# Kernel optimization log

Measured on AMD Instinct MI355X. Metric: run time of the kernel, lower is better.

## Reference

```python
import jax, jax.numpy as jnp
import numpy as np

OBS_LEN = 20   # decoder timesteps
NC = 2         # n_coordinates
D = 64         # z_dim + s_dim (LSTM hidden size)
K = 20         # number of latent samples (len(pred_lstm_hidden))
N = 50000      # number of agents
H_MID = 32     # mapping MLP hidden dim


def setup_inputs() -> dict:
    key = jax.random.key(0)
    ks = jax.random.split(key, 8)
    return {
        "obs_traj_rel": jax.random.normal(ks[0], (OBS_LEN, N, NC), jnp.float32),
        "pred_lstm_hidden": jax.random.normal(ks[1], (K, N, D), jnp.float32),
        # mapping MLP: Linear(D->32) + LeakyReLU, Linear(32->D)
        "map_w1": jax.random.normal(ks[2], (H_MID, D), jnp.float32) * 0.1,
        "map_b1": jnp.zeros((H_MID,), jnp.float32),
        "map_w2": jax.random.normal(ks[3], (D, H_MID), jnp.float32) * 0.1,
        "map_b2": jnp.zeros((D,), jnp.float32),
        # LSTMCell params (weights ~ N(0, 0.1), biases zero per _initialize_weights)
        "w_ih": jax.random.normal(ks[4], (4 * D, NC), jnp.float32) * 0.1,
        "w_hh": jax.random.normal(ks[5], (4 * D, D), jnp.float32) * 0.1,
        "b_ih": jnp.zeros((4 * D,), jnp.float32),
        "b_hh": jnp.zeros((4 * D,), jnp.float32),
        # pred_hidden2pos: Linear(D -> NC)
        "pos_w": jax.random.normal(ks[6], (NC, D), jnp.float32) * 0.1,
        "pos_b": jnp.zeros((NC,), jnp.float32),
    }


def _hardsigmoid(x):
    # F.hardsigmoid: relu6(x + 3) / 6
    return jnp.clip(x / 6.0 + 0.5, 0.0, 1.0)


def _hardtanh(x):
    return jnp.clip(x, -1.0, 1.0)


def reference(obs_traj_rel, pred_lstm_hidden, map_w1, map_b1, map_w2, map_b2,
              w_ih, w_hh, b_ih, b_hh, pos_w, pos_b):
    # mapping MLP on initial hidden state: [K, N, D]
    h0 = jax.nn.leaky_relu(pred_lstm_hidden @ map_w1.T + map_b1, negative_slope=0.01)
    h0 = h0 @ map_w2.T + map_b2
    c0 = jnp.zeros_like(h0)

    # input at step i uses obs_traj_rel[max(i-1, 0)]
    idx = jnp.concatenate([jnp.zeros((1,), jnp.int32),
                           jnp.arange(OBS_LEN - 1, dtype=jnp.int32)])
    xs = obs_traj_rel[idx, :, :NC]  # [T, N, NC]

    def step(carry, x_t):
        h, c = carry                                   # [K, N, D]
        xb = jnp.broadcast_to(x_t, (K,) + x_t.shape)   # repeat over samples
        gates = xb @ w_ih.T + b_ih + h @ w_hh.T + b_hh  # [K, N, 4D]
        i_g, f_g, g_g, o_g = jnp.split(gates, 4, axis=-1)
        c_new = _hardsigmoid(f_g) * c + _hardsigmoid(i_g) * _hardtanh(g_g)
        h_new = _hardsigmoid(o_g) * _hardtanh(c_new)
        out = h_new @ pos_w.T + pos_b                  # [K, N, NC]
        return (h_new, c_new), out

    _, outs = jax.lax.scan(step, (h0, c0), xs)
    return outs  # [T, K, N, NC]
```

## Files before the change

kernel.cpp:

```cpp
#include <hip/hip_runtime.h>

#define T_STEPS 20
#define KK      20
#define NW      50000
#define DD      64

typedef __attribute__((ext_vector_type(8))) short bfx8;
typedef __attribute__((ext_vector_type(4))) short sx4;
typedef __attribute__((ext_vector_type(4))) float fx4;

__device__ __forceinline__ short f2bf(float f){
  unsigned u = __builtin_bit_cast(unsigned, f);
  return (short)((u + 0x7FFFu + ((u >> 16) & 1u)) >> 16);
}
__device__ __forceinline__ float hsig(float x){ return fminf(fmaxf(fmaf(x, 0.16666667f, 0.5f), 0.f), 1.f); }
__device__ __forceinline__ float htanh(float x){ return fminf(fmaxf(x, -1.f), 1.f); }

__device__ __forceinline__ bfx8 frag_f32(const float* p0, const float* p1){
  fx4 lo = *(const fx4*)p0, hi = *(const fx4*)p1;
  bfx8 r;
  r[0]=f2bf(lo[0]); r[1]=f2bf(lo[1]); r[2]=f2bf(lo[2]); r[3]=f2bf(lo[3]);
  r[4]=f2bf(hi[0]); r[5]=f2bf(hi[1]); r[6]=f2bf(hi[2]); r[7]=f2bf(hi[3]);
  return r;
}
__device__ __forceinline__ bfx8 frag_lds(const unsigned short* p0, const unsigned short* p1){
  sx4 lo = *(const sx4*)p0, hi = *(const sx4*)p1;
  bfx8 r;
  r[0]=lo[0]; r[1]=lo[1]; r[2]=lo[2]; r[3]=lo[3];
  r[4]=hi[0]; r[5]=hi[1]; r[6]=hi[2]; r[7]=hi[3];
  return r;
}

__global__ __launch_bounds__(256)
void gcrl_fused(const float* __restrict__ obs, const float* __restrict__ pred,
                const float* __restrict__ w1, const float* __restrict__ b1,
                const float* __restrict__ w2, const float* __restrict__ b2,
                const float* __restrict__ wih, const float* __restrict__ whh,
                const float* __restrict__ bih, const float* __restrict__ bhh,
                const float* __restrict__ posw, const float* __restrict__ posb,
                float* __restrict__ out)
{
  __shared__ unsigned short hbuf[2][16][72];
  __shared__ unsigned short l1buf[16][36];
  __shared__ float xs[19][4][2];

  const int tid = threadIdx.x;
  const int w   = tid >> 6;
  const int l   = tid & 63;
  const int g   = l >> 4;
  const int cc  = l & 15;

  const int bid = blockIdx.x;
  const int k0  = (bid % 5) * 4;
  const int n0  = (bid / 5) * 4;

  for (int i = tid; i < 19 * 8; i += 256){
    int row = i >> 3, r = i & 7;
    xs[row][r >> 1][r & 1] = obs[(size_t)row * (NW * 2) + (size_t)(n0 + (r >> 1)) * 2 + (r & 1)];
  }

  bfx8 wf[4][2];
  float wx0[4], wx1[4], bsum[4];
  #pragma unroll
  for (int ty = 0; ty < 4; ++ty){
    const int j = ty * 64 + w * 16 + cc;
    wx0[ty]  = wih[j * 2 + 0];
    wx1[ty]  = wih[j * 2 + 1];
    bsum[ty] = bih[j] + bhh[j];
    #pragma unroll
    for (int kt = 0; kt < 2; ++kt)
      wf[ty][kt] = frag_f32(&whh[j * DD + kt * 32 + g * 4],
                            &whh[j * DD + kt * 32 + 16 + g * 4]);
  }

  const int c2 = (cc < 2) ? cc : 0;
  bfx8 pf[2];
  #pragma unroll
  for (int kt = 0; kt < 2; ++kt)
    pf[kt] = frag_f32(&posw[c2 * DD + kt * 32 + g * 4],
                      &posw[c2 * DD + kt * 32 + 16 + g * 4]);
  const float pbias = posb[c2];

  {
    const int kcell = k0 + (cc & 3);
    const int ncell = n0 + (cc >> 2);
    const float* Pr = pred + ((size_t)kcell * NW + ncell) * DD;
    bfx8 pa0 = frag_f32(&Pr[g * 4],      &Pr[16 + g * 4]);
    bfx8 pa1 = frag_f32(&Pr[32 + g * 4], &Pr[48 + g * 4]);
    if (w == 0){
      #pragma unroll
      for (int nt = 0; nt < 2; ++nt){
        const int j1 = nt * 16 + cc;
        bfx8 bf0 = frag_f32(&w1[j1 * DD + g * 4],      &w1[j1 * DD + 16 + g * 4]);
        bfx8 bf1 = frag_f32(&w1[j1 * DD + 32 + g * 4], &w1[j1 * DD + 48 + g * 4]);
        const float bb = b1[j1];
        fx4 acc = {bb, bb, bb, bb};
        acc = __builtin_amdgcn_mfma_f32_16x16x32_bf16(pa0, bf0, acc, 0, 0, 0);
        acc = __builtin_amdgcn_mfma_f32_16x16x32_bf16(pa1, bf1, acc, 0, 0, 0);
        #pragma unroll
        for (int r = 0; r < 4; ++r){
          float xv = acc[r];
          l1buf[g * 4 + r][nt * 16 + cc] =
            (unsigned short)f2bf(fmaxf(xv, 0.f) + 0.01f * fminf(xv, 0.f));
        }
      }
    }
  }
  __syncthreads();
  {
    bfx8 a2 = frag_lds(&l1buf[cc][g * 4], &l1buf[cc][16 + g * 4]);
    const int j2 = w * 16 + cc;
    bfx8 b2f = frag_f32(&w2[j2 * 32 + g * 4], &w2[j2 * 32 + 16 + g * 4]);
    const float bb = b2[j2];
    fx4 acc = {bb, bb, bb, bb};
    acc = __builtin_amdgcn_mfma_f32_16x16x32_bf16(a2, b2f, acc, 0, 0, 0);
    #pragma unroll
    for (int r = 0; r < 4; ++r)
      hbuf[0][g * 4 + r][w * 16 + cc] = (unsigned short)f2bf(acc[r]);
  }
  float cst[4] = {0.f, 0.f, 0.f, 0.f};
  __syncthreads();

  #pragma unroll 2
  for (int t = 0; t < T_STEPS; ++t){
    const int xi = (t == 0) ? 0 : (t - 1);
    const float x0v = xs[xi][g][0];
    const float x1v = xs[xi][g][1];

    const unsigned short* hrow = &hbuf[t & 1][cc][0];
    bfx8 ha0 = frag_lds(&hrow[g * 4],      &hrow[16 + g * 4]);
    bfx8 ha1 = frag_lds(&hrow[32 + g * 4], &hrow[48 + g * 4]);

    fx4 acc[4];
    #pragma unroll
    for (int ty = 0; ty < 4; ++ty){
      const float xv = fmaf(wx0[ty], x0v, fmaf(wx1[ty], x1v, bsum[ty]));
      fx4 a = {xv, xv, xv, xv};
      a = __builtin_amdgcn_mfma_f32_16x16x32_bf16(ha0, wf[ty][0], a, 0, 0, 0);
      a = __builtin_amdgcn_mfma_f32_16x16x32_bf16(ha1, wf[ty][1], a, 0, 0, 0);
      acc[ty] = a;
    }

    if (w == 0 && t > 0){
      fx4 oa = {pbias, pbias, pbias, pbias};
      oa = __builtin_amdgcn_mfma_f32_16x16x32_bf16(ha0, pf[0], oa, 0, 0, 0);
      oa = __builtin_amdgcn_mfma_f32_16x16x32_bf16(ha1, pf[1], oa, 0, 0, 0);
      if (cc < 2){
        #pragma unroll
        for (int r = 0; r < 4; ++r)
          out[(((size_t)(t - 1) * KK + (k0 + r)) * NW + (n0 + g)) * 2 + cc] = oa[r];
      }
    }

    #pragma unroll
    for (int r = 0; r < 4; ++r){
      const float iv = acc[0][r], fv = acc[1][r], gv = acc[2][r], ov = acc[3][r];
      const float cn = fmaf(hsig(fv), cst[r], hsig(iv) * htanh(gv));
      cst[r] = cn;
      hbuf[(t + 1) & 1][g * 4 + r][w * 16 + cc] = (unsigned short)f2bf(hsig(ov) * htanh(cn));
    }
    __syncthreads();
  }

  if (w == 0){
    const unsigned short* hrow = &hbuf[0][cc][0];
    bfx8 ha0 = frag_lds(&hrow[g * 4],      &hrow[16 + g * 4]);
    bfx8 ha1 = frag_lds(&hrow[32 + g * 4], &hrow[48 + g * 4]);
    fx4 oa = {pbias, pbias, pbias, pbias};
    oa = __builtin_amdgcn_mfma_f32_16x16x32_bf16(ha0, pf[0], oa, 0, 0, 0);
    oa = __builtin_amdgcn_mfma_f32_16x16x32_bf16(ha1, pf[1], oa, 0, 0, 0);
    if (cc < 2){
      #pragma unroll
      for (int r = 0; r < 4; ++r)
        out[(((size_t)19 * KK + (k0 + r)) * NW + (n0 + g)) * 2 + cc] = oa[r];
    }
  }
}

extern "C" void kernel_launch(void* const* d_in, const int* in_sizes, int n_in,
                              void* d_out, int out_size, void* d_ws, size_t ws_size,
                              hipStream_t stream){
  const float* obs  = (const float*)d_in[0];
  const float* pred = (const float*)d_in[1];
  const float* w1   = (const float*)d_in[2];
  const float* b1   = (const float*)d_in[3];
  const float* w2   = (const float*)d_in[4];
  const float* b2   = (const float*)d_in[5];
  const float* wih  = (const float*)d_in[6];
  const float* whh  = (const float*)d_in[7];
  const float* bih  = (const float*)d_in[8];
  const float* bhh  = (const float*)d_in[9];
  const float* posw = (const float*)d_in[10];
  const float* posb = (const float*)d_in[11];
  float* o = (float*)d_out;

  dim3 grid((NW / 4) * (KK / 4));
  dim3 block(256);
  gcrl_fused<<<grid, block, 0, stream>>>(obs, pred, w1, b1, w2, b2,
                                         wih, whh, bih, bhh, posw, posb, o);
}
```

Baseline: 1.279 ms.

## Process two cell tiles per block with transposed MFMA and packed bf16 LDS traffic

Each block now covers 8 agents instead of 4, giving two independent 16-cell tiles whose MFMA chains interleave per step. The gate MFMA is transposed so weights are operand A, which lets the bias be preloaded as a per-register accumulator and h be stored as packed vectors. The input projection moves into an extra MFMA with a zero-padded bf16 operand. Other changes: v_cvt_pk_bf16_f32 packing, fmed3 clamps, a manually unrolled double-buffered loop, and vectorized output stores. The aim is to halve barriers per cell and hide MFMA latency. In exchange there are more registers per thread, fewer blocks, and the x input is now rounded to bf16.

```diff
diff --git a/kernel.cpp b/kernel.cpp
--- a/kernel.cpp
+++ b/kernel.cpp
@@ -8,13 +8,23 @@
 typedef __attribute__((ext_vector_type(8))) short bfx8;
 typedef __attribute__((ext_vector_type(4))) short sx4;
 typedef __attribute__((ext_vector_type(4))) float fx4;
+typedef __attribute__((ext_vector_type(2))) float fx2;
+typedef __attribute__((ext_vector_type(2))) int   ix2;
+typedef __attribute__((ext_vector_type(4))) int   ix4;
 
 __device__ __forceinline__ short f2bf(float f){
   unsigned u = __builtin_bit_cast(unsigned, f);
   return (short)((u + 0x7FFFu + ((u >> 16) & 1u)) >> 16);
 }
-__device__ __forceinline__ float hsig(float x){ return fminf(fmaxf(fmaf(x, 0.16666667f, 0.5f), 0.f), 1.f); }
-__device__ __forceinline__ float htanh(float x){ return fminf(fmaxf(x, -1.f), 1.f); }
+__device__ __forceinline__ unsigned cvtpk(float lo, float hi){
+  unsigned r; asm("v_cvt_pk_bf16_f32 %0, %1, %2" : "=v"(r) : "v"(lo), "v"(hi)); return r;
+}
+__device__ __forceinline__ float hsig(float x){
+  return __builtin_amdgcn_fmed3f(fmaf(x, 0.16666667f, 0.5f), 0.f, 1.f);
+}
+__device__ __forceinline__ float htanh(float x){
+  return __builtin_amdgcn_fmed3f(x, -1.f, 1.f);
+}
 
 __device__ __forceinline__ bfx8 frag_f32(const float* p0, const float* p1){
   fx4 lo = *(const fx4*)p0, hi = *(const fx4*)p1;
@@ -30,6 +40,12 @@
   r[4]=hi[0]; r[5]=hi[1]; r[6]=hi[2]; r[7]=hi[3];
   return r;
 }
+__device__ __forceinline__ bfx8 cat(ix2 lo, ix2 hi){
+  ix4 t; t[0]=lo[0]; t[1]=lo[1]; t[2]=hi[0]; t[3]=hi[1];
+  return __builtin_bit_cast(bfx8, t);
+}
+
+#define MFMA(A,B,C) __builtin_amdgcn_mfma_f32_16x16x32_bf16((A),(B),(C),0,0,0)
 
 __global__ __launch_bounds__(256)
 void gcrl_fused(const float* __restrict__ obs, const float* __restrict__ pred,
@@ -40,9 +56,9 @@
                 const float* __restrict__ posw, const float* __restrict__ posb,
                 float* __restrict__ out)
 {
-  __shared__ unsigned short hbuf[2][16][72];
-  __shared__ unsigned short l1buf[16][36];
-  __shared__ float xs[19][4][2];
+  __shared__ unsigned short hst[2][2][1152];
+  __shared__ unsigned short l1buf[2][16][36];
+  __shared__ float xs[19][8][2];
 
   const int tid = threadIdx.x;
   const int w   = tid >> 6;
@@ -52,129 +68,170 @@
 
   const int bid = blockIdx.x;
   const int k0  = (bid % 5) * 4;
-  const int n0  = (bid / 5) * 4;
-
-  for (int i = tid; i < 19 * 8; i += 256){
-    int row = i >> 3, r = i & 7;
-    xs[row][r >> 1][r & 1] = obs[(size_t)row * (NW * 2) + (size_t)(n0 + (r >> 1)) * 2 + (r & 1)];
+  const int n0  = (bid / 5) * 8;
+
+  for (int i = tid; i < 19 * 16; i += 256){
+    int row = i >> 4, rr = i & 15;
+    xs[row][rr >> 1][rr & 1] =
+      obs[(size_t)row * (NW * 2) + (size_t)(n0 + (rr >> 1)) * 2 + (rr & 1)];
   }
 
   bfx8 wf[4][2];
-  float wx0[4], wx1[4], bsum[4];
+  bfx8 a2f[4];
+  fx4  bs[4];
   #pragma unroll
   for (int ty = 0; ty < 4; ++ty){
-    const int j = ty * 64 + w * 16 + cc;
-    wx0[ty]  = wih[j * 2 + 0];
-    wx1[ty]  = wih[j * 2 + 1];
-    bsum[ty] = bih[j] + bhh[j];
+    const int jrow = ty * 64 + w * 16 + cc;
     #pragma unroll
     for (int kt = 0; kt < 2; ++kt)
-      wf[ty][kt] = frag_f32(&whh[j * DD + kt * 32 + g * 4],
-                            &whh[j * DD + kt * 32 + 16 + g * 4]);
-  }
-
+      wf[ty][kt] = frag_f32(&whh[jrow * DD + kt * 32 + g * 4],
+                            &whh[jrow * DD + kt * 32 + 16 + g * 4]);
+    unsigned xw = cvtpk(wih[jrow * 2 + 0], wih[jrow * 2 + 1]);
+    ix4 t4; t4[0] = (g == 0) ? (int)xw : 0; t4[1] = 0; t4[2] = 0; t4[3] = 0;
+    a2f[ty] = __builtin_bit_cast(bfx8, t4);
+    const int jreg = ty * 64 + w * 16 + g * 4;
+    bs[ty][0] = bih[jreg + 0] + bhh[jreg + 0];
+    bs[ty][1] = bih[jreg + 1] + bhh[jreg + 1];
+    bs[ty][2] = bih[jreg + 2] + bhh[jreg + 2];
+    bs[ty][3] = bih[jreg + 3] + bhh[jreg + 3];
+  }
   const int c2 = (cc < 2) ? cc : 0;
   bfx8 pf[2];
   #pragma unroll
   for (int kt = 0; kt < 2; ++kt)
     pf[kt] = frag_f32(&posw[c2 * DD + kt * 32 + g * 4],
                       &posw[c2 * DD + kt * 32 + 16 + g * 4]);
-  const float pbias = posb[c2];
-
-  {
+  fx4 pC; pC[0] = posb[0]; pC[1] = posb[1]; pC[2] = 0.f; pC[3] = 0.f;
+
+  float* const outBase =
+    out + ((size_t)(k0 + (cc & 3)) * NW + n0 + w * 4 + (cc >> 2)) * 2;
+
+  if (w < 2){
+    const int tl = w;
     const int kcell = k0 + (cc & 3);
-    const int ncell = n0 + (cc >> 2);
+    const int ncell = n0 + tl * 4 + (cc >> 2);
     const float* Pr = pred + ((size_t)kcell * NW + ncell) * DD;
     bfx8 pa0 = frag_f32(&Pr[g * 4],      &Pr[16 + g * 4]);
     bfx8 pa1 = frag_f32(&Pr[32 + g * 4], &Pr[48 + g * 4]);
-    if (w == 0){
+    #pragma unroll
+    for (int nt = 0; nt < 2; ++nt){
+      const int j1 = nt * 16 + cc;
+      bfx8 bf0 = frag_f32(&w1[j1 * DD + g * 4],      &w1[j1 * DD + 16 + g * 4]);
+      bfx8 bf1 = frag_f32(&w1[j1 * DD + 32 + g * 4], &w1[j1 * DD + 48 + g * 4]);
+      const float bb = b1[j1];
+      fx4 acc = {bb, bb, bb, bb};
+      acc = MFMA(pa0, bf0, acc);
+      acc = MFMA(pa1, bf1, acc);
       #pragma unroll
-      for (int nt = 0; nt < 2; ++nt){
-        const int j1 = nt * 16 + cc;
-        bfx8 bf0 = frag_f32(&w1[j1 * DD + g * 4],      &w1[j1 * DD + 16 + g * 4]);
-        bfx8 bf1 = frag_f32(&w1[j1 * DD + 32 + g * 4], &w1[j1 * DD + 48 + g * 4]);
-        const float bb = b1[j1];
-        fx4 acc = {bb, bb, bb, bb};
-        acc = __builtin_amdgcn_mfma_f32_16x16x32_bf16(pa0, bf0, acc, 0, 0, 0);
-        acc = __builtin_amdgcn_mfma_f32_16x16x32_bf16(pa1, bf1, acc, 0, 0, 0);
-        #pragma unroll
-        for (int r = 0; r < 4; ++r){
-          float xv = acc[r];
-          l1buf[g * 4 + r][nt * 16 + cc] =
-            (unsigned short)f2bf(fmaxf(xv, 0.f) + 0.01f * fminf(xv, 0.f));
-        }
+      for (int r = 0; r < 4; ++r){
+        float xv = acc[r];
+        l1buf[tl][g * 4 + r][nt * 16 + cc] =
+          (unsigned short)f2bf(fmaxf(xv, 0.f) + 0.01f * fminf(xv, 0.f));
       }
     }
   }
   __syncthreads();
-  {
-    bfx8 a2 = frag_lds(&l1buf[cc][g * 4], &l1buf[cc][16 + g * 4]);
-    const int j2 = w * 16 + cc;
-    bfx8 b2f = frag_f32(&w2[j2 * 32 + g * 4], &w2[j2 * 32 + 16 + g * 4]);
-    const float bb = b2[j2];
-    fx4 acc = {bb, bb, bb, bb};
-    acc = __builtin_amdgcn_mfma_f32_16x16x32_bf16(a2, b2f, acc, 0, 0, 0);
-    #pragma unroll
-    for (int r = 0; r < 4; ++r)
-      hbuf[0][g * 4 + r][w * 16 + cc] = (unsigned short)f2bf(acc[r]);
-  }
-  float cst[4] = {0.f, 0.f, 0.f, 0.f};
+
+  #pragma unroll
+  for (int tl = 0; tl < 2; ++tl){
+    bfx8 bfr = frag_lds(&l1buf[tl][cc][g * 4], &l1buf[tl][cc][16 + g * 4]);
+    bfx8 afr = frag_f32(&w2[(w * 16 + cc) * 32 + g * 4],
+                        &w2[(w * 16 + cc) * 32 + 16 + g * 4]);
+    const int d0 = w * 16 + g * 4;
+    fx4 ci; ci[0] = b2[d0]; ci[1] = b2[d0 + 1]; ci[2] = b2[d0 + 2]; ci[3] = b2[d0 + 3];
+    fx4 acc = MFMA(afr, bfr, ci);
+    ix2 pk;
+    pk[0] = (int)cvtpk(acc[0], acc[1]);
+    pk[1] = (int)cvtpk(acc[2], acc[3]);
+    *(ix2*)&hst[0][tl][cc * 72 + w * 16 + g * 4] = pk;
+  }
+  float cA0=0.f,cA1=0.f,cA2=0.f,cA3=0.f, cB0=0.f,cB1=0.f,cB2=0.f,cB3=0.f;
   __syncthreads();
 
-  #pragma unroll 2
-  for (int t = 0; t < T_STEPS; ++t){
-    const int xi = (t == 0) ? 0 : (t - 1);
-    const float x0v = xs[xi][g][0];
-    const float x1v = xs[xi][g][1];
-
-    const unsigned short* hrow = &hbuf[t & 1][cc][0];
-    bfx8 ha0 = frag_lds(&hrow[g * 4],      &hrow[16 + g * 4]);
-    bfx8 ha1 = frag_lds(&hrow[32 + g * 4], &hrow[48 + g * 4]);
-
-    fx4 acc[4];
-    #pragma unroll
-    for (int ty = 0; ty < 4; ++ty){
-      const float xv = fmaf(wx0[ty], x0v, fmaf(wx1[ty], x1v, bsum[ty]));
-      fx4 a = {xv, xv, xv, xv};
-      a = __builtin_amdgcn_mfma_f32_16x16x32_bf16(ha0, wf[ty][0], a, 0, 0, 0);
-      a = __builtin_amdgcn_mfma_f32_16x16x32_bf16(ha1, wf[ty][1], a, 0, 0, 0);
-      acc[ty] = a;
+  const unsigned short* const rb = &hst[0][0][cc * 72 + g * 4];
+  unsigned short*       const wb = &hst[0][0][cc * 72 + w * 16 + g * 4];
+
+#define STEP(XI, TPREV, DOPROJ, RB, WB) do{                                    \
+    const int xi_ = (XI);                                                      \
+    const fx2 xA = *(const fx2*)&xs[xi_][cc >> 2][0];                          \
+    const fx2 xB = *(const fx2*)&xs[xi_][4 + (cc >> 2)][0];                    \
+    ix2 lA0 = *(const ix2*)(RB);         ix2 hA0 = *(const ix2*)((RB) + 16);   \
+    ix2 lA1 = *(const ix2*)((RB) + 32);  ix2 hA1 = *(const ix2*)((RB) + 48);   \
+    ix2 lB0 = *(const ix2*)((RB) + 1152);ix2 hB0 = *(const ix2*)((RB) + 1168); \
+    ix2 lB1 = *(const ix2*)((RB) + 1184);ix2 hB1 = *(const ix2*)((RB) + 1200); \
+    bfx8 hbA0 = cat(lA0, hA0), hbA1 = cat(lA1, hA1);                           \
+    bfx8 hbB0 = cat(lB0, hB0), hbB1 = cat(lB1, hB1);                           \
+    unsigned uA = cvtpk(xA[0], xA[1]);                                         \
+    unsigned uB = cvtpk(xB[0], xB[1]);                                         \
+    ix4 tA4; tA4[0] = (g == 0) ? (int)uA : 0; tA4[1]=0; tA4[2]=0; tA4[3]=0;    \
+    ix4 tB4; tB4[0] = (g == 0) ? (int)uB : 0; tB4[1]=0; tB4[2]=0; tB4[3]=0;    \
+    bfx8 xbA = __builtin_bit_cast(bfx8, tA4);                                  \
+    bfx8 xbB = __builtin_bit_cast(bfx8, tB4);                                  \
+    fx4 accA[4], accB[4];                                                      \
+    _Pragma("unroll")                                                          \
+    for (int ty = 0; ty < 4; ++ty){                                            \
+      fx4 aa = MFMA(wf[ty][0], hbA0, bs[ty]);                                  \
+      aa = MFMA(wf[ty][1], hbA1, aa);                                          \
+      aa = MFMA(a2f[ty], xbA, aa);                                             \
+      accA[ty] = aa;                                                           \
+      fx4 ab = MFMA(wf[ty][0], hbB0, bs[ty]);                                  \
+      ab = MFMA(wf[ty][1], hbB1, ab);                                          \
+      ab = MFMA(a2f[ty], xbB, ab);                                             \
+      accB[ty] = ab;                                                           \
+    }                                                                          \
+    if ((DOPROJ) && w < 2){                                                    \
+      bfx8 h0 = w ? hbB0 : hbA0;                                               \
+      bfx8 h1 = w ? hbB1 : hbA1;                                               \
+      fx4 oa = MFMA(pf[0], h0, pC);                                            \
+      oa = MFMA(pf[1], h1, oa);                                                \
+      if (g == 0){                                                             \
+        fx2 ov; ov[0] = oa[0]; ov[1] = oa[1];                                  \
+        *(fx2*)(outBase + (size_t)(TPREV) * (KK * NW * 2)) = ov;               \
+      }                                                                        \
+    }                                                                          \
+    {                                                                          \
+      float cn0 = fmaf(hsig(accA[1][0]), cA0, hsig(accA[0][0])*htanh(accA[2][0])); \
+      float cn1 = fmaf(hsig(accA[1][1]), cA1, hsig(accA[0][1])*htanh(accA[2][1])); \
+      float cn2 = fmaf(hsig(accA[1][2]), cA2, hsig(accA[0][2])*htanh(accA[2][2])); \
+      float cn3 = fmaf(hsig(accA[1][3]), cA3, hsig(accA[0][3])*htanh(accA[2][3])); \
+      cA0=cn0; cA1=cn1; cA2=cn2; cA3=cn3;                                      \
+      ix2 pk;                                                                  \
+      pk[0] = (int)cvtpk(hsig(accA[3][0])*htanh(cn0), hsig(accA[3][1])*htanh(cn1)); \
+      pk[1] = (int)cvtpk(hsig(accA[3][2])*htanh(cn2), hsig(accA[3][3])*htanh(cn3)); \
+      *(ix2*)(WB) = pk;                                                        \
+    }                                                                          \
+    {                                                                          \
+      float cn0 = fmaf(hsig(accB[1][0]), cB0, hsig(accB[0][0])*htanh(accB[2][0])); \
+      float cn1 = fmaf(hsig(accB[1][1]), cB1, hsig(accB[0][1])*htanh(accB[2][1])); \
+      float cn2 = fmaf(hsig(accB[1][2]), cB2, hsig(accB[0][2])*htanh(accB[2][2])); \
+      float cn3 = fmaf(hsig(accB[1][3]), cB3, hsig(accB[0][3])*htanh(accB[2][3])); \
+      cB0=cn0; cB1=cn1; cB2=cn2; cB3=cn3;                                      \
+      ix2 pk;                                                                  \
+      pk[0] = (int)cvtpk(hsig(accB[3][0])*htanh(cn0), hsig(accB[3][1])*htanh(cn1)); \
+      pk[1] = (int)cvtpk(hsig(accB[3][2])*htanh(cn2), hsig(accB[3][3])*htanh(cn3)); \
+      *(ix2*)((WB) + 1152) = pk;                                               \
+    }                                                                          \
+    __syncthreads();                                                           \
+  }while(0)
+
+  for (int t = 0; t < T_STEPS; t += 2){
+    STEP((t == 0 ? 0 : t - 1), t - 1, (t > 0), rb,        wb + 2304);
+    STEP(t,                    t,     1,       rb + 2304, wb);
+  }
+
+  if (w < 2){
+    const unsigned short* eb = rb + w * 1152;
+    ix2 l0 = *(const ix2*)eb,        h0 = *(const ix2*)(eb + 16);
+    ix2 l1 = *(const ix2*)(eb + 32), h1 = *(const ix2*)(eb + 48);
+    bfx8 hb0 = cat(l0, h0), hb1 = cat(l1, h1);
+    fx4 oa = MFMA(pf[0], hb0, pC);
+    oa = MFMA(pf[1], hb1, oa);
+    if (g == 0){
+      fx2 ov; ov[0] = oa[0]; ov[1] = oa[1];
+      *(fx2*)(outBase + (size_t)19 * (KK * NW * 2)) = ov;
     }
-
-    if (w == 0 && t > 0){
-      fx4 oa = {pbias, pbias, pbias, pbias};
-      oa = __builtin_amdgcn_mfma_f32_16x16x32_bf16(ha0, pf[0], oa, 0, 0, 0);
-      oa = __builtin_amdgcn_mfma_f32_16x16x32_bf16(ha1, pf[1], oa, 0, 0, 0);
-      if (cc < 2){
-        #pragma unroll
-        for (int r = 0; r < 4; ++r)
-          out[(((size_t)(t - 1) * KK + (k0 + r)) * NW + (n0 + g)) * 2 + cc] = oa[r];
-      }
-    }
-
-    #pragma unroll
-    for (int r = 0; r < 4; ++r){
-      const float iv = acc[0][r], fv = acc[1][r], gv = acc[2][r], ov = acc[3][r];
-      const float cn = fmaf(hsig(fv), cst[r], hsig(iv) * htanh(gv));
-      cst[r] = cn;
-      hbuf[(t + 1) & 1][g * 4 + r][w * 16 + cc] = (unsigned short)f2bf(hsig(ov) * htanh(cn));
-    }
-    __syncthreads();
-  }
-
-  if (w == 0){
-    const unsigned short* hrow = &hbuf[0][cc][0];
-    bfx8 ha0 = frag_lds(&hrow[g * 4],      &hrow[16 + g * 4]);
-    bfx8 ha1 = frag_lds(&hrow[32 + g * 4], &hrow[48 + g * 4]);
-    fx4 oa = {pbias, pbias, pbias, pbias};
-    oa = __builtin_amdgcn_mfma_f32_16x16x32_bf16(ha0, pf[0], oa, 0, 0, 0);
-    oa = __builtin_amdgcn_mfma_f32_16x16x32_bf16(ha1, pf[1], oa, 0, 0, 0);
-    if (cc < 2){
-      #pragma unroll
-      for (int r = 0; r < 4; ++r)
-        out[(((size_t)19 * KK + (k0 + r)) * NW + (n0 + g)) * 2 + cc] = oa[r];
-    }
-  }
+  }
+#undef STEP
 }
 
 extern "C" void kernel_launch(void* const* d_in, const int* in_sizes, int n_in,
@@ -194,7 +251,7 @@
   const float* posb = (const float*)d_in[11];
   float* o = (float*)d_out;
 
-  dim3 grid((NW / 4) * (KK / 4));
+  dim3 grid(5 * (NW / 8));
   dim3 block(256);
   gcrl_fused<<<grid, block, 0, stream>>>(obs, pred, w1, b1, w2, b2,
                                          wih, whh, bih, bhh, posw, posb, o);
```

Result: faster. 1.174 ms (-8.2%).
